# Performance work log

Measured on AMD Instinct MI355X. Metric: run time of the kernel, lower is better.

## Reference

```python
import jax, jax.numpy as jnp
import numpy as np
from jax.scipy.special import erf

# ---- physical constants (scipy.constants values; FIELD_CONSTANT in eV*Angstrom per e^2) ----
E_CHARGE = 1.602176634e-19
EPS0 = 8.8541878128e-12
PI = float(np.pi)
FIELD_CONSTANT = E_CHARGE * 1e10 / EPS0          # e/(eps0) with Angstrom length units
K_COUL = FIELD_CONSTANT / (4.0 * PI)             # ~14.3996 eV*A

# ---- module hyperparameters (from init_kwargs) ----
SIGMA_D = 0.5
SIGMAS = np.array([0.4, 0.8, 1.2, 1.6], dtype=np.float32)
NUM_RADIAL = 4
OFFSET = 0.1
N_PER_GRAPH = 128
NUM_GRAPHS = 32
M_NODES = N_PER_GRAPH * NUM_GRAPHS

# total_width_factors = sqrt((sigma_d^2 + sigma_r^2)/2)
W_FACTORS = np.sqrt((SIGMA_D**2 + SIGMAS**2) / 2.0).astype(np.float32)      # [R]
# multipole-normalized GTO: C_l = 1/(2^{l+1/2} sigma^{2l+3} Gamma(l+3/2)) => C1/C0 = 1/(3 sigma^2)
L0_FACTORS = np.ones(NUM_RADIAL, dtype=np.float32)                          # ratio = 1 under 'multipoles'
L1_FACTORS = (np.sqrt(3.0) * SIGMAS**2 * (1.0 / (3.0 * SIGMAS**2)) / OFFSET).astype(np.float32)

# 7 duplicate offsets: center, +x, +y, +z, -x, -y, -z
_h = OFFSET
OFFSETS7 = np.array([[0,0,0],[_h,0,0],[0,_h,0],[0,0,_h],[-_h,0,0],[0,-_h,0],[0,0,-_h]], dtype=np.float32)


def _duplicate_charges(sf):
    # sf: [M,4] -> [M,7] FD charge assignment (matches torch slot layout)
    t = 2.0 * OFFSET
    s0, s1, s2, s3 = sf[:, 0], sf[:, 1], sf[:, 2], sf[:, 3]
    return jnp.stack([s0, s3 / t, s1 / t, s2 / t, -s3 / t, -s1 / t, -s2 / t], axis=1)


def _project(sf7):
    # sf7: [M,7,R] per-duplicate scalar features -> [M, 4R]
    M = sf7.shape[0]
    l0 = jnp.asarray(L0_FACTORS) * sf7[:, 0]                                 # [M,R]
    half = 0.5 * jnp.asarray(L1_FACTORS)
    vy = half * (sf7[:, 2] - sf7[:, 5])   # column offset 0 in each triplet
    vz = half * (sf7[:, 3] - sf7[:, 6])   # column offset 1
    vx = half * (sf7[:, 1] - sf7[:, 4])   # column offset 2
    l1 = jnp.stack([vy, vz, vx], axis=-1).reshape(M, 3 * NUM_RADIAL)         # interleaved per radial
    return jnp.concatenate([l0, l1], axis=1)                                 # [M,4R]


def setup_inputs() -> dict:
    key = jax.random.key(0)
    k1, k2 = jax.random.split(key)
    source_feats = jax.random.normal(k1, (M_NODES, 1, 4), dtype=jnp.float32)
    node_positions = 4.0 * jax.random.normal(k2, (M_NODES, 3), dtype=jnp.float32)  # ~Angstrom scale
    batch = jnp.repeat(jnp.arange(NUM_GRAPHS, dtype=jnp.int64), N_PER_GRAPH)
    return {"source_feats": source_feats, "node_positions": node_positions, "batch": batch}


def reference(source_feats, node_positions, batch):
    # density_max_l=1, projection_max_l=1 -> call_density_1_feats_1 path.
    # Assumes equal-size graphs: batch = repeat(arange(G), n) (enforced by setup_inputs).
    sf = source_feats[:, 0, :]                                               # squeeze(-2): [M,4]
    M = sf.shape[0]
    G, n, D, R = NUM_GRAPHS, N_PER_GRAPH, 7 * N_PER_GRAPH, NUM_RADIAL
    w = jnp.asarray(W_FACTORS)                                               # [R]

    charges = _duplicate_charges(sf)                                         # [M,7]
    pos7 = node_positions[:, None, :] + jnp.asarray(OFFSETS7)[None]          # [M,7,3]

    pg = pos7.reshape(G, D, 3)
    cg = charges.reshape(G, D)

    diff = pg[:, :, None, :] - pg[:, None, :, :]                             # [G,D,D,3]
    d2 = jnp.sum(diff * diff, axis=-1)                                       # [G,D,D]
    orig = jnp.arange(D) // 7
    mask = (orig[:, None] != orig[None, :])                                  # exclude same-original-node pairs
    d = jnp.sqrt(jnp.where(mask, d2, 1.0))                                   # safe sqrt (masked entries dummy)
    smooth = erf(0.5 * d[..., None] / w) / (d[..., None] + 1e-6)             # [G,D,D,R]
    smooth = smooth * mask[None, :, :, None]
    # scatter_sum over senders i into receivers j
    sfeat = K_COUL * jnp.einsum('gi,gijr->gjr', cg, smooth)                  # [G,D,R]
    sfeat = sfeat.reshape(M, 7, R)

    # GTOSelfInteractionBlock (reconstructed): interactions among a node's own
    # 7 duplicates with analytic d->0 limit erf(x)/x -> 1/(w*sqrt(pi)).
    off = jnp.asarray(OFFSETS7)
    ds = jnp.linalg.norm(off[:, None, :] - off[None, :, :], axis=-1)          # [7,7]
    phi = jnp.where(ds[..., None] > 0.0,
                    erf(0.5 * ds[..., None] / w) / (ds[..., None] + 1e-6),
                    1.0 / (w * np.sqrt(PI)))                                  # [7,7,R]
    sself = K_COUL * jnp.einsum('mi,ijr->mjr', charges, phi)                  # [M,7,R]

    features = _project(sfeat)
    self_terms = _project(sself)
    features = features + self_terms                                          # include_self_interaction=True
    return features, self_terms
```

## Files before the change

kernel.cpp:

```cpp
#include <hip/hip_runtime.h>
#include <math.h>

namespace {


constexpr int   MTOT = 4096;
constexpr float H    = 0.1f;

constexpr float W0 = 0.45276925690687087f;
constexpr float W1 = 0.66708320320631664f;
constexpr float W2 = 0.91923881554251174f;
constexpr float W3 = 1.18532695911296985f;

constexpr float KCOUL   = 14.399645478425669f;
constexpr float HALF_L1 = 2.8867513459481287f;
constexpr float SQRTPI  = 1.7724538509055159f;

constexpr float PK[4] = {0.5195472f, 0.3526314f, 0.2559019f, 0.1984558f};
constexpr float C2[4] = {-1.7593842f, -0.8105028f, -0.4268329f, -0.2567073f};
constexpr float EA1 = 0.3480242f, EA2 = -0.0958798f, EA3 = 0.7478556f;
constexpr float RCP_H = 9.9999000f, RCP_HS2 = 7.0710178f, RCP_2H = 4.9999750f;

constexpr float KA[4]  = {1.2460860f, 0.84575637f, 0.61375334f, 0.47597746f};
constexpr float K2X[4] = {2.4390243f, 1.1235959f, 0.59171598f, 0.35587189f};

constexpr float NEAR2   = 6.25f;
constexpr int   NEARCAP = 256;

__device__ __forceinline__ float fast_rcp(float x)  { return __builtin_amdgcn_rcpf(x); }
__device__ __forceinline__ float fast_rsq(float x)  { return __builtin_amdgcn_rsqf(x); }
__device__ __forceinline__ float fast_exp2(float x) { return __builtin_amdgcn_exp2f(x); }

__device__ __forceinline__ float erf_q(float d, float d2, float pk, float c2) {
  float t = fast_rcp(__builtin_fmaf(d, pk, 1.0f));
  float poly = t * __builtin_fmaf(t, __builtin_fmaf(t, EA3, EA2), EA1);
  return poly * fast_exp2(d2 * c2);
}

__device__ __forceinline__ float project_one(const float* S, int k) {
  if (k < 4) return S[k];
  int q = k - 4;
  int r = q / 3;
  int comp = q - 3 * r;
  int j1, j2;
  if (comp == 0)      { j1 = 2; j2 = 5; }
  else if (comp == 1) { j1 = 3; j2 = 6; }
  else                { j1 = 1; j2 = 4; }
  return HALF_L1 * (S[j1 * 4 + r] - S[j2 * 4 + r]);
}

__device__ __forceinline__ float offx(int a) { return (a == 1) ? H : (a == 4) ? -H : 0.0f; }
__device__ __forceinline__ float offy(int a) { return (a == 2) ? H : (a == 5) ? -H : 0.0f; }
__device__ __forceinline__ float offz(int a) { return (a == 3) ? H : (a == 6) ? -H : 0.0f; }

__global__ __launch_bounds__(256, 4) void es_main(
    const float* __restrict__ sf,
    const float* __restrict__ pos,
    float* __restrict__ out)
{
  __shared__ float4 s_pos4[128];
  __shared__ float4 s_chg4[128];
  __shared__ float  s_red[4][16];
  __shared__ float  s_nearS[4][7][4];
  __shared__ int    s_nearI[NEARCAP];
  __shared__ int    s_ncnt;
  __shared__ float  s_feat[4 * 28];
  __shared__ float  s_self[4 * 28];

  const int b   = blockIdx.x;
  const int g   = b >> 5;
  const int grp = b & 31;
  const int tid = threadIdx.x;
  const int t   = tid >> 6;
  const int c   = tid & 63;

  if (tid < 128) {
    const float* p = pos + (size_t)(g * 128 + tid) * 3;
    const float4 s = ((const float4*)sf)[g * 128 + tid];
    s_pos4[tid] = make_float4(p[0], p[1], p[2], 0.0f);
    s_chg4[tid] = make_float4(s.x, 5.0f * s.w, 5.0f * s.y, 5.0f * s.z);
  }
  if (tid < 112) ((float*)s_nearS)[tid] = 0.0f;
  if (tid == 0) s_ncnt = 0;
  __syncthreads();

  const int own = grp * 4 + t;
  const float4 cp = s_pos4[own];

  float acc[16];
#pragma unroll
  for (int k = 0; k < 16; ++k) acc[k] = 0.0f;

#pragma unroll
  for (int si = 0; si < 2; ++si) {
    const int j = c + 64 * si;
    if (j != own) {
      const float4 p4 = s_pos4[j];
      const float4 c4 = s_chg4[j];
      const float vx = cp.x - p4.x;
      const float vy = cp.y - p4.y;
      const float vz = cp.z - p4.z;
      const float d2 = __builtin_fmaf(vx, vx, __builtin_fmaf(vy, vy, vz * vz));
      if (d2 < NEAR2) {
        int slot = atomicAdd(&s_ncnt, 1);
        if (slot < NEARCAP) s_nearI[slot] = (t << 8) | j;
      } else {
        const float rd  = fast_rsq(d2);
        const float d   = d2 * rd;
        const float rd2 = rd * rd;
        const float rd3 = rd2 * rd;
        const float rd4 = rd2 * rd2;
        const float S3  = 3.0f * rd3;
        const float S4  = 3.0f * rd4;
        const float dot = __builtin_fmaf(c4.y, vx, __builtin_fmaf(c4.z, vy, c4.w * vz));
        const float dp  = 0.2f * dot;
        const float c0  = c4.x;
#pragma unroll
        for (int r = 0; r < 4; ++r) {
          const float tt = fast_rcp(__builtin_fmaf(d, PK[r], 1.0f));
          const float X  = fast_exp2(d2 * C2[r]);
          const float q  = tt * __builtin_fmaf(tt, __builtin_fmaf(tt, EA3, EA2), EA1) * X;
          const float E  = 1.0f - q;
          const float A  = KA[r] * X;
          const float gv = E * rd;
          const float gp = (A - gv) * rd;
          const float Bv = -gp * rd;
          const float h1 = __builtin_fmaf(K2X[r], rd, S3);
          const float Bp = __builtin_fmaf(A, h1, -(E * S4));
          acc[r] = __builtin_fmaf(dp, Bv, __builtin_fmaf(c0, gv, acc[r]));
          const float sv  = __builtin_fmaf(dp, Bp, c0 * gp) * rd;
          const float B02 = 0.2f * Bv;
          acc[4 + r]  = __builtin_fmaf(sv, vx, __builtin_fmaf(B02, c4.y, acc[4 + r]));
          acc[8 + r]  = __builtin_fmaf(sv, vy, __builtin_fmaf(B02, c4.z, acc[8 + r]));
          acc[12 + r] = __builtin_fmaf(sv, vz, __builtin_fmaf(B02, c4.w, acc[12 + r]));
        }
      }
    }
  }

#pragma unroll
  for (int k = 0; k < 16; ++k) {
    float v = acc[k];
    v += __shfl_xor(v, 1);
    v += __shfl_xor(v, 2);
    v += __shfl_xor(v, 4);
    v += __shfl_xor(v, 8);
    v += __shfl_xor(v, 16);
    v += __shfl_xor(v, 32);
    acc[k] = v;
  }
  if (c == 0) {
#pragma unroll
    for (int k = 0; k < 16; ++k) s_red[t][k] = acc[k];
  }
  __syncthreads();

  const int N = (s_ncnt < NEARCAP) ? s_ncnt : NEARCAP;
  for (int e = t; e < N; e += 4) {
    const int ent = s_nearI[e];
    const int tt  = ent >> 8;
    const int j   = ent & 127;
    const int a   = c >> 3;
    const int i   = c & 7;
    const bool act = (a < 7) && (i < 7);
    const float4 tp = s_pos4[grp * 4 + tt];
    const float4 p4 = s_pos4[j];
    const float4 c4 = s_chg4[j];
    const float ci = !act ? 0.0f :
                     (i == 0) ?  c4.x : (i == 1) ?  c4.y : (i == 2) ?  c4.z :
                     (i == 3) ?  c4.w : (i == 4) ? -c4.y : (i == 5) ? -c4.z : -c4.w;
    const float sx = tp.x - p4.x + offx(a) - offx(i);
    const float sy = tp.y - p4.y + offy(a) - offy(i);
    const float sz = tp.z - p4.z + offz(a) - offz(i);
    const float d2 = fmaxf(__builtin_fmaf(sx, sx, __builtin_fmaf(sy, sy, sz * sz)), 1e-12f);
    const float rd = fast_rsq(d2);
    const float d  = d2 * rd;
    const float cv = ci * rd;
    float vr[4];
#pragma unroll
    for (int r = 0; r < 4; ++r) {
      const float tt2 = fast_rcp(__builtin_fmaf(d, PK[r], 1.0f));
      const float q   = tt2 * __builtin_fmaf(tt2, __builtin_fmaf(tt2, EA3, EA2), EA1)
                            * fast_exp2(d2 * C2[r]);
      vr[r] = cv * (1.0f - q);
    }
#pragma unroll
    for (int r = 0; r < 4; ++r) {
      float v = vr[r];
      v += __shfl_xor(v, 1);
      v += __shfl_xor(v, 2);
      v += __shfl_xor(v, 4);
      vr[r] = v;
    }
    if (i == 0 && a < 7) {
#pragma unroll
      for (int r = 0; r < 4; ++r) atomicAdd(&s_nearS[tt][a][r], vr[r]);
    }
  }
  __syncthreads();

  if (tid < 112) {
    const int node = tid / 28;
    const int rem  = tid - node * 28;
    const int a    = rem >> 2;
    const int r    = rem & 3;

    const float pot = s_red[node][r];
    const float gx  = s_red[node][4 + r];
    const float gy  = s_red[node][8 + r];
    const float gz  = s_red[node][12 + r];
    const float od  = (a == 1) ?  H * gx : (a == 2) ?  H * gy : (a == 3) ?  H * gz :
                      (a == 4) ? -H * gx : (a == 5) ? -H * gy : (a == 6) ? -H * gz : 0.0f;
    const float mid = pot + od + s_nearS[node][a][r];

    const float w  = (r == 0) ? W0 : (r == 1) ? W1 : (r == 2) ? W2 : W3;
    const float pk = PK[r];
    const float c2 = C2[r];
    const float diag = fast_rcp(w * SQRTPI);
    const float ph1 = (1.f - erf_q(0.1f,        0.01f, pk, c2)) * RCP_H;
    const float ph2 = (1.f - erf_q(0.14142136f, 0.02f, pk, c2)) * RCP_HS2;
    const float ph3 = (1.f - erf_q(0.2f,        0.04f, pk, c2)) * RCP_2H;

    const float4 c4 = s_chg4[grp * 4 + node];
    float selfSum = 0.f;
#pragma unroll
    for (int i = 0; i < 7; ++i) {
      const float ci = (i == 0) ?  c4.x : (i == 1) ?  c4.y : (i == 2) ?  c4.z :
                       (i == 3) ?  c4.w : (i == 4) ? -c4.y : (i == 5) ? -c4.z : -c4.w;
      float ph;
      if (i == a)                            ph = diag;
      else if (i == 0 || a == 0)             ph = ph1;
      else if ((i - a == 3) || (a - i == 3)) ph = ph3;
      else                                   ph = ph2;
      selfSum = __builtin_fmaf(ci, ph, selfSum);
    }
    const float sv = KCOUL * selfSum;
    s_self[tid] = sv;
    s_feat[tid] = __builtin_fmaf(KCOUL, mid, sv);
  }
  __syncthreads();

  if (tid < 64) {
    const int node = tid >> 4;
    const int k    = tid & 15;
    const int m    = g * 128 + grp * 4 + node;
    out[m * 16 + k]             = project_one(&s_feat[node * 28], k);
    out[MTOT * 16 + m * 16 + k] = project_one(&s_self[node * 28], k);
  }
}

}

extern "C" void kernel_launch(void* const* d_in, const int* in_sizes, int n_in,
                              void* d_out, int out_size, void* d_ws, size_t ws_size,
                              hipStream_t stream) {
  const float* sf  = (const float*)d_in[0];
  const float* pos = (const float*)d_in[1];
  float* out = (float*)d_out;
  es_main<<<1024, 256, 0, stream>>>(sf, pos, out);
}
```

Baseline: 69.55 us.

## Use one wavefront per node with register/shuffle-based reductions instead of shared memory

The kernel moves from 256-thread blocks covering four nodes to 64-thread single-wavefront blocks covering one node each. All shared memory, atomics and block barriers go away: the near-pair list becomes a wave ballot loop that broadcasts each near source with shuffles and processes it immediately, and the final reduction and projection use cross-lane shuffles. Positions and charges are read straight from global memory (cached) rather than staged in LDS. The cost is four times as many blocks and uniform per-wave serialization of the near-pair loop.

```diff
diff --git a/kernel.cpp b/kernel.cpp
--- a/kernel.cpp
+++ b/kernel.cpp
@@ -24,8 +24,7 @@
 constexpr float KA[4]  = {1.2460860f, 0.84575637f, 0.61375334f, 0.47597746f};
 constexpr float K2X[4] = {2.4390243f, 1.1235959f, 0.59171598f, 0.35587189f};
 
-constexpr float NEAR2   = 6.25f;
-constexpr int   NEARCAP = 256;
+constexpr float NEAR2 = 6.25f;
 
 __device__ __forceinline__ float fast_rcp(float x)  { return __builtin_amdgcn_rcpf(x); }
 __device__ __forceinline__ float fast_rsq(float x)  { return __builtin_amdgcn_rsqf(x); }
@@ -37,103 +36,116 @@
   return poly * fast_exp2(d2 * c2);
 }
 
-__device__ __forceinline__ float project_one(const float* S, int k) {
-  if (k < 4) return S[k];
-  int q = k - 4;
-  int r = q / 3;
-  int comp = q - 3 * r;
-  int j1, j2;
-  if (comp == 0)      { j1 = 2; j2 = 5; }
-  else if (comp == 1) { j1 = 3; j2 = 6; }
-  else                { j1 = 1; j2 = 4; }
-  return HALF_L1 * (S[j1 * 4 + r] - S[j2 * 4 + r]);
-}
-
 __device__ __forceinline__ float offx(int a) { return (a == 1) ? H : (a == 4) ? -H : 0.0f; }
 __device__ __forceinline__ float offy(int a) { return (a == 2) ? H : (a == 5) ? -H : 0.0f; }
 __device__ __forceinline__ float offz(int a) { return (a == 3) ? H : (a == 6) ? -H : 0.0f; }
 
-__global__ __launch_bounds__(256, 4) void es_main(
+__global__ __launch_bounds__(64, 4) void es_main(
     const float* __restrict__ sf,
     const float* __restrict__ pos,
     float* __restrict__ out)
 {
-  __shared__ float4 s_pos4[128];
-  __shared__ float4 s_chg4[128];
-  __shared__ float  s_red[4][16];
-  __shared__ float  s_nearS[4][7][4];
-  __shared__ int    s_nearI[NEARCAP];
-  __shared__ int    s_ncnt;
-  __shared__ float  s_feat[4 * 28];
-  __shared__ float  s_self[4 * 28];
-
-  const int b   = blockIdx.x;
-  const int g   = b >> 5;
-  const int grp = b & 31;
-  const int tid = threadIdx.x;
-  const int t   = tid >> 6;
-  const int c   = tid & 63;
-
-  if (tid < 128) {
-    const float* p = pos + (size_t)(g * 128 + tid) * 3;
-    const float4 s = ((const float4*)sf)[g * 128 + tid];
-    s_pos4[tid] = make_float4(p[0], p[1], p[2], 0.0f);
-    s_chg4[tid] = make_float4(s.x, 5.0f * s.w, 5.0f * s.y, 5.0f * s.z);
-  }
-  if (tid < 112) ((float*)s_nearS)[tid] = 0.0f;
-  if (tid == 0) s_ncnt = 0;
-  __syncthreads();
-
-  const int own = grp * 4 + t;
-  const float4 cp = s_pos4[own];
+  const int b    = blockIdx.x;
+  const int base = b & ~127;
+  const int c    = threadIdx.x;
+
+  const float tx = pos[(size_t)b * 3 + 0];
+  const float ty = pos[(size_t)b * 3 + 1];
+  const float tz = pos[(size_t)b * 3 + 2];
+  const float4 os = ((const float4*)sf)[b];
+  const float4 oc = make_float4(os.x, 5.0f * os.w, 5.0f * os.y, 5.0f * os.z);
 
   float acc[16];
 #pragma unroll
   for (int k = 0; k < 16; ++k) acc[k] = 0.0f;
+  float nacc0 = 0.f, nacc1 = 0.f, nacc2 = 0.f, nacc3 = 0.f;
+
+  const int a_sub = c >> 3;
+  const int i_sub = c & 7;
 
 #pragma unroll
   for (int si = 0; si < 2; ++si) {
-    const int j = c + 64 * si;
-    if (j != own) {
-      const float4 p4 = s_pos4[j];
-      const float4 c4 = s_chg4[j];
-      const float vx = cp.x - p4.x;
-      const float vy = cp.y - p4.y;
-      const float vz = cp.z - p4.z;
-      const float d2 = __builtin_fmaf(vx, vx, __builtin_fmaf(vy, vy, vz * vz));
-      if (d2 < NEAR2) {
-        int slot = atomicAdd(&s_ncnt, 1);
-        if (slot < NEARCAP) s_nearI[slot] = (t << 8) | j;
-      } else {
-        const float rd  = fast_rsq(d2);
-        const float d   = d2 * rd;
-        const float rd2 = rd * rd;
-        const float rd3 = rd2 * rd;
-        const float rd4 = rd2 * rd2;
-        const float S3  = 3.0f * rd3;
-        const float S4  = 3.0f * rd4;
-        const float dot = __builtin_fmaf(c4.y, vx, __builtin_fmaf(c4.z, vy, c4.w * vz));
-        const float dp  = 0.2f * dot;
-        const float c0  = c4.x;
-#pragma unroll
-        for (int r = 0; r < 4; ++r) {
-          const float tt = fast_rcp(__builtin_fmaf(d, PK[r], 1.0f));
-          const float X  = fast_exp2(d2 * C2[r]);
-          const float q  = tt * __builtin_fmaf(tt, __builtin_fmaf(tt, EA3, EA2), EA1) * X;
-          const float E  = 1.0f - q;
-          const float A  = KA[r] * X;
-          const float gv = E * rd;
-          const float gp = (A - gv) * rd;
-          const float Bv = -gp * rd;
-          const float h1 = __builtin_fmaf(K2X[r], rd, S3);
-          const float Bp = __builtin_fmaf(A, h1, -(E * S4));
-          acc[r] = __builtin_fmaf(dp, Bv, __builtin_fmaf(c0, gv, acc[r]));
-          const float sv  = __builtin_fmaf(dp, Bp, c0 * gp) * rd;
-          const float B02 = 0.2f * Bv;
-          acc[4 + r]  = __builtin_fmaf(sv, vx, __builtin_fmaf(B02, c4.y, acc[4 + r]));
-          acc[8 + r]  = __builtin_fmaf(sv, vy, __builtin_fmaf(B02, c4.z, acc[8 + r]));
-          acc[12 + r] = __builtin_fmaf(sv, vz, __builtin_fmaf(B02, c4.w, acc[12 + r]));
-        }
+    const int j = base + c + 64 * si;
+    const float px = pos[(size_t)j * 3 + 0];
+    const float py = pos[(size_t)j * 3 + 1];
+    const float pz = pos[(size_t)j * 3 + 2];
+    const float4 s4 = ((const float4*)sf)[j];
+    const float cx = s4.x, cy = 5.0f * s4.w, cz = 5.0f * s4.y, cw = 5.0f * s4.z;
+
+    const float vx = tx - px;
+    const float vy = ty - py;
+    const float vz = tz - pz;
+    const float d2 = __builtin_fmaf(vx, vx, __builtin_fmaf(vy, vy, vz * vz));
+    const bool self  = (j == b);
+    const bool nearp = (d2 < NEAR2) && !self;
+
+    if (!self && !nearp) {
+      const float rd  = fast_rsq(d2);
+      const float d   = d2 * rd;
+      const float rd2 = rd * rd;
+      const float rd3 = rd2 * rd;
+      const float rd4 = rd2 * rd2;
+      const float S3  = 3.0f * rd3;
+      const float S4  = 3.0f * rd4;
+      const float dot = __builtin_fmaf(cy, vx, __builtin_fmaf(cz, vy, cw * vz));
+      const float dp  = 0.2f * dot;
+#pragma unroll
+      for (int r = 0; r < 4; ++r) {
+        const float tt = fast_rcp(__builtin_fmaf(d, PK[r], 1.0f));
+        const float X  = fast_exp2(d2 * C2[r]);
+        const float q  = tt * __builtin_fmaf(tt, __builtin_fmaf(tt, EA3, EA2), EA1) * X;
+        const float E  = 1.0f - q;
+        const float A  = KA[r] * X;
+        const float gv = E * rd;
+        const float gp = (A - gv) * rd;
+        const float Bv = -gp * rd;
+        const float h1 = __builtin_fmaf(K2X[r], rd, S3);
+        const float Bp = __builtin_fmaf(A, h1, -(E * S4));
+        acc[r] = __builtin_fmaf(dp, Bv, __builtin_fmaf(cx, gv, acc[r]));
+        const float sv  = __builtin_fmaf(dp, Bp, cx * gp) * rd;
+        const float B02 = 0.2f * Bv;
+        acc[4 + r]  = __builtin_fmaf(sv, vx, __builtin_fmaf(B02, cy, acc[4 + r]));
+        acc[8 + r]  = __builtin_fmaf(sv, vy, __builtin_fmaf(B02, cz, acc[8 + r]));
+        acc[12 + r] = __builtin_fmaf(sv, vz, __builtin_fmaf(B02, cw, acc[12 + r]));
+      }
+    }
+
+    unsigned long long m = __ballot(nearp);
+    while (m) {
+      const int src = __ffsll(m) - 1;
+      m &= m - 1;
+      const float qx = __shfl(px, src), qy = __shfl(py, src), qz = __shfl(pz, src);
+      const float bx = __shfl(cx, src), by = __shfl(cy, src);
+      const float bz = __shfl(cz, src), bw = __shfl(cw, src);
+      const bool act = (a_sub < 7) && (i_sub < 7);
+      const float ci = !act ? 0.0f :
+                       (i_sub == 0) ?  bx : (i_sub == 1) ?  by : (i_sub == 2) ?  bz :
+                       (i_sub == 3) ?  bw : (i_sub == 4) ? -by : (i_sub == 5) ? -bz : -bw;
+      const float sx = tx - qx + offx(a_sub) - offx(i_sub);
+      const float sy = ty - qy + offy(a_sub) - offy(i_sub);
+      const float sz = tz - qz + offz(a_sub) - offz(i_sub);
+      const float dn2 = fmaxf(__builtin_fmaf(sx, sx, __builtin_fmaf(sy, sy, sz * sz)), 1e-12f);
+      const float rdn = fast_rsq(dn2);
+      const float dn  = dn2 * rdn;
+      const float cv  = ci * rdn;
+      float vr[4];
+#pragma unroll
+      for (int r = 0; r < 4; ++r) {
+        const float tt = fast_rcp(__builtin_fmaf(dn, PK[r], 1.0f));
+        const float q  = tt * __builtin_fmaf(tt, __builtin_fmaf(tt, EA3, EA2), EA1)
+                            * fast_exp2(dn2 * C2[r]);
+        vr[r] = cv * (1.0f - q);
+      }
+#pragma unroll
+      for (int r = 0; r < 4; ++r) {
+        float v = vr[r];
+        v += __shfl_xor(v, 1);
+        v += __shfl_xor(v, 2);
+        v += __shfl_xor(v, 4);
+        vr[r] = v;
+      }
+      if (i_sub == 0) {
+        nacc0 += vr[0]; nacc1 += vr[1]; nacc2 += vr[2]; nacc3 += vr[3];
       }
     }
   }
@@ -149,104 +161,68 @@
     v += __shfl_xor(v, 32);
     acc[k] = v;
   }
-  if (c == 0) {
-#pragma unroll
-    for (int k = 0; k < 16; ++k) s_red[t][k] = acc[k];
-  }
-  __syncthreads();
-
-  const int N = (s_ncnt < NEARCAP) ? s_ncnt : NEARCAP;
-  for (int e = t; e < N; e += 4) {
-    const int ent = s_nearI[e];
-    const int tt  = ent >> 8;
-    const int j   = ent & 127;
-    const int a   = c >> 3;
-    const int i   = c & 7;
-    const bool act = (a < 7) && (i < 7);
-    const float4 tp = s_pos4[grp * 4 + tt];
-    const float4 p4 = s_pos4[j];
-    const float4 c4 = s_chg4[j];
-    const float ci = !act ? 0.0f :
-                     (i == 0) ?  c4.x : (i == 1) ?  c4.y : (i == 2) ?  c4.z :
-                     (i == 3) ?  c4.w : (i == 4) ? -c4.y : (i == 5) ? -c4.z : -c4.w;
-    const float sx = tp.x - p4.x + offx(a) - offx(i);
-    const float sy = tp.y - p4.y + offy(a) - offy(i);
-    const float sz = tp.z - p4.z + offz(a) - offz(i);
-    const float d2 = fmaxf(__builtin_fmaf(sx, sx, __builtin_fmaf(sy, sy, sz * sz)), 1e-12f);
-    const float rd = fast_rsq(d2);
-    const float d  = d2 * rd;
-    const float cv = ci * rd;
-    float vr[4];
-#pragma unroll
-    for (int r = 0; r < 4; ++r) {
-      const float tt2 = fast_rcp(__builtin_fmaf(d, PK[r], 1.0f));
-      const float q   = tt2 * __builtin_fmaf(tt2, __builtin_fmaf(tt2, EA3, EA2), EA1)
-                            * fast_exp2(d2 * C2[r]);
-      vr[r] = cv * (1.0f - q);
-    }
-#pragma unroll
-    for (int r = 0; r < 4; ++r) {
-      float v = vr[r];
-      v += __shfl_xor(v, 1);
-      v += __shfl_xor(v, 2);
-      v += __shfl_xor(v, 4);
-      vr[r] = v;
-    }
-    if (i == 0 && a < 7) {
-#pragma unroll
-      for (int r = 0; r < 4; ++r) atomicAdd(&s_nearS[tt][a][r], vr[r]);
-    }
-  }
-  __syncthreads();
-
-  if (tid < 112) {
-    const int node = tid / 28;
-    const int rem  = tid - node * 28;
-    const int a    = rem >> 2;
-    const int r    = rem & 3;
-
-    const float pot = s_red[node][r];
-    const float gx  = s_red[node][4 + r];
-    const float gy  = s_red[node][8 + r];
-    const float gz  = s_red[node][12 + r];
-    const float od  = (a == 1) ?  H * gx : (a == 2) ?  H * gy : (a == 3) ?  H * gz :
-                      (a == 4) ? -H * gx : (a == 5) ? -H * gy : (a == 6) ? -H * gz : 0.0f;
-    const float mid = pot + od + s_nearS[node][a][r];
-
-    const float w  = (r == 0) ? W0 : (r == 1) ? W1 : (r == 2) ? W2 : W3;
-    const float pk = PK[r];
-    const float c2 = C2[r];
-    const float diag = fast_rcp(w * SQRTPI);
-    const float ph1 = (1.f - erf_q(0.1f,        0.01f, pk, c2)) * RCP_H;
-    const float ph2 = (1.f - erf_q(0.14142136f, 0.02f, pk, c2)) * RCP_HS2;
-    const float ph3 = (1.f - erf_q(0.2f,        0.04f, pk, c2)) * RCP_2H;
-
-    const float4 c4 = s_chg4[grp * 4 + node];
-    float selfSum = 0.f;
-#pragma unroll
-    for (int i = 0; i < 7; ++i) {
-      const float ci = (i == 0) ?  c4.x : (i == 1) ?  c4.y : (i == 2) ?  c4.z :
-                       (i == 3) ?  c4.w : (i == 4) ? -c4.y : (i == 5) ? -c4.z : -c4.w;
-      float ph;
-      if (i == a)                            ph = diag;
-      else if (i == 0 || a == 0)             ph = ph1;
-      else if ((i - a == 3) || (a - i == 3)) ph = ph3;
-      else                                   ph = ph2;
-      selfSum = __builtin_fmaf(ci, ph, selfSum);
-    }
-    const float sv = KCOUL * selfSum;
-    s_self[tid] = sv;
-    s_feat[tid] = __builtin_fmaf(KCOUL, mid, sv);
-  }
-  __syncthreads();
-
-  if (tid < 64) {
-    const int node = tid >> 4;
-    const int k    = tid & 15;
-    const int m    = g * 128 + grp * 4 + node;
-    out[m * 16 + k]             = project_one(&s_feat[node * 28], k);
-    out[MTOT * 16 + m * 16 + k] = project_one(&s_self[node * 28], k);
-  }
+
+  const int l = (c < 28) ? c : 0;
+  const int a = l >> 2;
+  const int r = l & 3;
+
+  const float pot = (r == 0) ? acc[0]  : (r == 1) ? acc[1]  : (r == 2) ? acc[2]  : acc[3];
+  const float gx  = (r == 0) ? acc[4]  : (r == 1) ? acc[5]  : (r == 2) ? acc[6]  : acc[7];
+  const float gy  = (r == 0) ? acc[8]  : (r == 1) ? acc[9]  : (r == 2) ? acc[10] : acc[11];
+  const float gz  = (r == 0) ? acc[12] : (r == 1) ? acc[13] : (r == 2) ? acc[14] : acc[15];
+
+  const float n0 = __shfl(nacc0, a * 8);
+  const float n1 = __shfl(nacc1, a * 8);
+  const float n2 = __shfl(nacc2, a * 8);
+  const float n3 = __shfl(nacc3, a * 8);
+  const float nearS = (r == 0) ? n0 : (r == 1) ? n1 : (r == 2) ? n2 : n3;
+
+  const float od = (a == 1) ?  H * gx : (a == 2) ?  H * gy : (a == 3) ?  H * gz :
+                   (a == 4) ? -H * gx : (a == 5) ? -H * gy : (a == 6) ? -H * gz : 0.0f;
+  const float mid = pot + od + nearS;
+
+  const float w   = (r == 0) ? W0    : (r == 1) ? W1    : (r == 2) ? W2    : W3;
+  const float pk  = (r == 0) ? PK[0] : (r == 1) ? PK[1] : (r == 2) ? PK[2] : PK[3];
+  const float c2v = (r == 0) ? C2[0] : (r == 1) ? C2[1] : (r == 2) ? C2[2] : C2[3];
+  const float diag = fast_rcp(w * SQRTPI);
+  const float ph1 = (1.f - erf_q(0.1f,        0.01f, pk, c2v)) * RCP_H;
+  const float ph2 = (1.f - erf_q(0.14142136f, 0.02f, pk, c2v)) * RCP_HS2;
+  const float ph3 = (1.f - erf_q(0.2f,        0.04f, pk, c2v)) * RCP_2H;
+
+  float selfSum = 0.f;
+#pragma unroll
+  for (int i = 0; i < 7; ++i) {
+    const float ci = (i == 0) ?  oc.x : (i == 1) ?  oc.y : (i == 2) ?  oc.z :
+                     (i == 3) ?  oc.w : (i == 4) ? -oc.y : (i == 5) ? -oc.z : -oc.w;
+    float ph;
+    if (i == a)                            ph = diag;
+    else if (i == 0 || a == 0)             ph = ph1;
+    else if ((i - a == 3) || (a - i == 3)) ph = ph3;
+    else                                   ph = ph2;
+    selfSum = __builtin_fmaf(ci, ph, selfSum);
+  }
+  const float selfv = KCOUL * selfSum;
+  const float featv = __builtin_fmaf(KCOUL, mid, selfv);
+
+  const int k = (c < 16) ? c : (c < 32 ? c - 16 : 0);
+  int idx1, idx2;
+  if (k < 4) {
+    idx1 = k; idx2 = 0;
+  } else {
+    const int q  = k - 4;
+    const int rr = q / 3;
+    const int comp = q - 3 * rr;
+    const int j1 = (comp == 0) ? 2 : (comp == 1) ? 3 : 1;
+    const int j2 = (comp == 0) ? 5 : (comp == 1) ? 6 : 4;
+    idx1 = j1 * 4 + rr; idx2 = j2 * 4 + rr;
+  }
+  const float f1 = __shfl(featv, idx1), f2 = __shfl(featv, idx2);
+  const float s1 = __shfl(selfv, idx1), s2 = __shfl(selfv, idx2);
+  const float F  = (k < 4) ? f1 : HALF_L1 * (f1 - f2);
+  const float S  = (k < 4) ? s1 : HALF_L1 * (s1 - s2);
+
+  if (c < 16)      out[(size_t)b * 16 + c] = F;
+  else if (c < 32) out[(size_t)MTOT * 16 + (size_t)b * 16 + (c - 16)] = S;
 }
 
 }
@@ -257,5 +233,5 @@
   const float* sf  = (const float*)d_in[0];
   const float* pos = (const float*)d_in[1];
   float* out = (float*)d_out;
-  es_main<<<1024, 256, 0, stream>>>(sf, pos, out);
-}
+  es_main<<<4096, 64, 0, stream>>>(sf, pos, out);
+}
```

After: 68.91 us. Within noise of the previous version (-0.9%).
